# Performance work log

Hardware: AMD Instinct MI355X
Metric: run time of the kernel (lower is better)

## Reference

```python
import jax, jax.numpy as jnp
import numpy as np

D_MODEL, D_KV, N_HEADS = 1024, 64, 16
NUM_BUCKETS, MAX_DIST = 32, 128
B, S = 2, 2048


def _relative_position_bucket(relative_position, num_buckets=NUM_BUCKETS, max_distance=MAX_DIST):
    # bidirectional=True branch of the TF code
    nb = num_buckets // 2
    n = -relative_position
    ret = (n < 0).astype(jnp.int32) * nb
    n = jnp.abs(n)
    max_exact = nb // 2
    is_small = n < max_exact
    val_if_large = max_exact + (
        jnp.log(n.astype(jnp.float32) / max_exact)
        / np.log(max_distance / max_exact)
        * (nb - max_exact)
    ).astype(jnp.int32)
    val_if_large = jnp.minimum(val_if_large, nb - 1)
    return ret + jnp.where(is_small, n, val_if_large)


def compute_bias(rel_emb, qlen, klen):
    ctx = jnp.arange(qlen)[:, None]
    mem = jnp.arange(klen)[None, :]
    rp_bucket = _relative_position_bucket(mem - ctx)  # [q, k]
    values = rel_emb[rp_bucket]                       # [q, k, h]
    return jnp.transpose(values, (2, 0, 1))[None]     # [1, h, q, k]


def setup_inputs() -> dict:
    key = jax.random.key(0)
    ks = jax.random.split(key, 6)
    sc = 1.0 / np.sqrt(D_MODEL)
    return {
        "inputs": jax.random.normal(ks[0], (B, S, D_MODEL), jnp.float32),
        "Wq": jax.random.normal(ks[1], (D_MODEL, N_HEADS * D_KV), jnp.float32) * sc,
        "Wk": jax.random.normal(ks[2], (D_MODEL, N_HEADS * D_KV), jnp.float32) * sc,
        "Wv": jax.random.normal(ks[3], (D_MODEL, N_HEADS * D_KV), jnp.float32) * sc,
        "Wo": jax.random.normal(ks[4], (N_HEADS * D_KV, D_MODEL), jnp.float32) * sc,
        "rel_emb": jax.random.normal(ks[5], (NUM_BUCKETS, N_HEADS), jnp.float32),
    }


def reference(inputs, Wq, Wk, Wv, Wo, rel_emb):
    bs, qlen, _ = inputs.shape

    def split_heads(x):
        return jnp.transpose(x.reshape(bs, -1, N_HEADS, D_KV), (0, 2, 1, 3))

    q = split_heads(inputs @ Wq)  # [b, h, s, d]
    k = split_heads(inputs @ Wk)
    v = split_heads(inputs @ Wv)

    position_bias = compute_bias(rel_emb, qlen, qlen)      # [1, h, q, k]
    scores = jnp.einsum('bnqd,bnkd->bnqk', q, k) + position_bias  # NOTE: no 1/sqrt(d) scaling (T5 style)
    attn = jax.nn.softmax(scores, axis=-1)
    hidden = jnp.einsum('bnqk,bnkd->bnqd', attn, v)
    hidden = jnp.transpose(hidden, (0, 2, 1, 3)).reshape(bs, qlen, N_HEADS * D_KV)
    return hidden @ Wo
```

## Files before the change

### kernel.cpp

```cpp
#include <hip/hip_runtime.h>


typedef __attribute__((ext_vector_type(8))) short s16x8;
typedef __attribute__((ext_vector_type(4))) float f32x4;
typedef __attribute__((ext_vector_type(16))) float f32x16;
typedef __attribute__((ext_vector_type(2))) unsigned int u32x2;

#if __has_builtin(__builtin_amdgcn_exp2f)
#define EXP2(x) __builtin_amdgcn_exp2f(x)
#else
#define EXP2(x) exp2f(x)
#endif

__device__ __forceinline__ unsigned short f2bf(float f) {
  unsigned int u = __float_as_uint(f);
  u = (u + 0x7fffu + ((u >> 16) & 1u)) >> 16;
  return (unsigned short)u;
}

__device__ __forceinline__ unsigned cvtpk(float lo, float hi) {
  unsigned r;
  asm("v_cvt_pk_bf16_f32 %0, %1, %2" : "=v"(r) : "v"(lo), "v"(hi));
  return r;
}

#define GLD16(g, l)                                              \
  __builtin_amdgcn_global_load_lds(                              \
      (const __attribute__((address_space(1))) void*)(g),        \
      (__attribute__((address_space(3))) void*)(l), 16, 0, 0)

__global__ __launch_bounds__(256) void cvt_lin(const float* __restrict__ in,
                                               unsigned short* __restrict__ out,
                                               int n4) {
  int i = blockIdx.x * 256 + threadIdx.x;
  int stride = gridDim.x * 256;
  for (; i < n4; i += stride) {
    float4 v = ((const float4*)in)[i];
    ushort4 o;
    o.x = f2bf(v.x); o.y = f2bf(v.y); o.z = f2bf(v.z); o.w = f2bf(v.w);
    ((ushort4*)out)[i] = o;
  }
}

__global__ __launch_bounds__(256) void cvt_prep(const float* __restrict__ W0,
                                                const float* __restrict__ W1,
                                                const float* __restrict__ W2,
                                                const float* __restrict__ W3,
                                                const float* __restrict__ rel,
                                                unsigned short* __restrict__ Dqkv,
                                                unsigned short* __restrict__ Do_,
                                                float* __restrict__ tab) {
  const int z = blockIdx.z;
  if (z == 4) {
    int idx = (blockIdx.y * 32 + blockIdx.x) * 256 + threadIdx.x;
    if (idx >= 16 * 4096) return;
    int h = idx >> 12, di = idx & 4095;
    int delta = di - 2047;
    int n = -delta;
    int ret = (n < 0) ? 16 : 0;
    n = n < 0 ? -n : n;
    int bucket;
    if (n < 8) {
      bucket = ret + n;
    } else {
      float lf = (float)log((double)n * 0.125);
      float f = lf / 2.772588722239781f * 8.0f;
      int v = 8 + (int)f;
      bucket = ret + (v < 15 ? v : 15);
    }
    tab[idx] = rel[bucket * 16 + h] * 1.4426950408889634f;
    return;
  }
  const float* W = (z == 0) ? W0 : (z == 1) ? W1 : (z == 2) ? W2 : W3;
  unsigned short* WT = (z < 3) ? (Dqkv + (size_t)z * 1024 * 1024) : Do_;
  __shared__ float t[32][33];
  int n0 = blockIdx.x * 32, k0 = blockIdx.y * 32;
  int tx = threadIdx.x & 31, ty = threadIdx.x >> 5;
#pragma unroll
  for (int i = 0; i < 32; i += 8)
    t[ty + i][tx] = W[(size_t)(k0 + ty + i) * 1024 + n0 + tx];
  __syncthreads();
#pragma unroll
  for (int i = 0; i < 32; i += 8)
    WT[(size_t)(n0 + ty + i) * 1024 + k0 + tx] = f2bf(t[tx][ty + i]);
}

__global__ __launch_bounds__(256, 2) void gemm_qkv(
    const unsigned short* __restrict__ A, const unsigned short* __restrict__ BT,
    unsigned short* __restrict__ O0, unsigned short* __restrict__ O1,
    unsigned short* __restrict__ O2) {
  __shared__ __align__(16) unsigned short aT[128 * 64];
  __shared__ __align__(16) unsigned short bT[128 * 64];
  const int tid = threadIdx.x;
  const int lane = tid & 63, w = tid >> 6;
  const int l15 = lane & 15, l4 = lane >> 4;
  const int m0 = blockIdx.y * 128, n0 = blockIdx.x * 128;
  const int wr = w >> 1, wc = w & 1;

  const f32x4 fzero = {0.f, 0.f, 0.f, 0.f};
  f32x4 acc[4][4];
#pragma unroll
  for (int i = 0; i < 4; ++i)
#pragma unroll
    for (int j = 0; j < 4; ++j) acc[i][j] = fzero;

  for (int k0 = 0; k0 < 1024; k0 += 64) {
#pragma unroll
    for (int p = 0; p < 4; ++p) {
      int slot = (p * 4 + w) * 64 + lane;
      int row = slot >> 3, s = slot & 7;
      int ks = (s ^ (row & 7)) << 3;
      GLD16(A + (size_t)(m0 + row) * 1024 + k0 + ks, (char*)aT + (p * 4 + w) * 1024);
      GLD16(BT + (size_t)(n0 + row) * 1024 + k0 + ks, (char*)bT + (p * 4 + w) * 1024);
    }
    __syncthreads();
#pragma unroll
    for (int kk = 0; kk < 2; ++kk) {
      int slotk = kk * 4 + l4;
      s16x8 af[4], bfr[4];
#pragma unroll
      for (int mi = 0; mi < 4; ++mi) {
        int row = wr * 64 + mi * 16 + l15;
        af[mi] = *(const s16x8*)(aT + row * 64 + ((slotk ^ (row & 7)) << 3));
      }
#pragma unroll
      for (int nj = 0; nj < 4; ++nj) {
        int row = wc * 64 + nj * 16 + l15;
        bfr[nj] = *(const s16x8*)(bT + row * 64 + ((slotk ^ (row & 7)) << 3));
      }
      __builtin_amdgcn_s_setprio(1);
#pragma unroll
      for (int mi = 0; mi < 4; ++mi)
#pragma unroll
        for (int nj = 0; nj < 4; ++nj)
          acc[mi][nj] = __builtin_amdgcn_mfma_f32_16x16x32_bf16(af[mi], bfr[nj], acc[mi][nj], 0, 0, 0);
      __builtin_amdgcn_s_setprio(0);
    }
    __syncthreads();
  }

#pragma unroll
  for (int mi = 0; mi < 4; ++mi)
#pragma unroll
    for (int nj = 0; nj < 4; ++nj)
#pragma unroll
      for (int r = 0; r < 4; ++r) {
        int row = m0 + wr * 64 + mi * 16 + l4 * 4 + r;
        int col = n0 + wc * 64 + nj * 16 + l15;
        int which = col >> 10;
        int cc = col & 1023;
        int b = row >> 11, s2 = row & 2047, hh = cc >> 6, d = cc & 63;
        if (which == 0)
          O0[((size_t)((b * 16 + hh) * 2048 + s2)) * 64 + d] =
              f2bf(acc[mi][nj][r] * 1.4426950408889634f);
        else if (which == 1)
          O1[((size_t)((b * 16 + hh) * 2048 + s2)) * 64 + d] = f2bf(acc[mi][nj][r]);
        else
          O2[((size_t)((b * 16 + hh) * 64 + d)) * 2048 + s2] = f2bf(acc[mi][nj][r]);
      }
}

__global__ __launch_bounds__(256, 2) void gemm_op(
    const unsigned short* __restrict__ A, const unsigned short* __restrict__ BT,
    float* __restrict__ O) {
  __shared__ __align__(16) unsigned short aT[128 * 64];
  __shared__ __align__(16) unsigned short bT[64 * 64];
  const int tid = threadIdx.x;
  const int lane = tid & 63, w = tid >> 6;
  const int l15 = lane & 15, l4 = lane >> 4;
  const int m0 = blockIdx.y * 128, n0 = blockIdx.x * 64;
  const int wr = w >> 1, wc = w & 1;

  const f32x4 fzero = {0.f, 0.f, 0.f, 0.f};
  f32x4 acc[4][2];
#pragma unroll
  for (int i = 0; i < 4; ++i)
#pragma unroll
    for (int j = 0; j < 2; ++j) acc[i][j] = fzero;

  for (int k0 = 0; k0 < 1024; k0 += 64) {
#pragma unroll
    for (int p = 0; p < 4; ++p) {
      int slot = (p * 4 + w) * 64 + lane;
      int row = slot >> 3, s = slot & 7;
      int ks = (s ^ (row & 7)) << 3;
      GLD16(A + (size_t)(m0 + row) * 1024 + k0 + ks, (char*)aT + (p * 4 + w) * 1024);
    }
#pragma unroll
    for (int p = 0; p < 2; ++p) {
      int slot = (p * 4 + w) * 64 + lane;
      int row = slot >> 3, s = slot & 7;
      int ks = (s ^ (row & 7)) << 3;
      GLD16(BT + (size_t)(n0 + row) * 1024 + k0 + ks, (char*)bT + (p * 4 + w) * 1024);
    }
    __syncthreads();
#pragma unroll
    for (int kk = 0; kk < 2; ++kk) {
      int slotk = kk * 4 + l4;
      s16x8 af[4], bfr[2];
#pragma unroll
      for (int mi = 0; mi < 4; ++mi) {
        int row = wr * 64 + mi * 16 + l15;
        af[mi] = *(const s16x8*)(aT + row * 64 + ((slotk ^ (row & 7)) << 3));
      }
#pragma unroll
      for (int nj = 0; nj < 2; ++nj) {
        int row = wc * 32 + nj * 16 + l15;
        bfr[nj] = *(const s16x8*)(bT + row * 64 + ((slotk ^ (row & 7)) << 3));
      }
      __builtin_amdgcn_s_setprio(1);
#pragma unroll
      for (int mi = 0; mi < 4; ++mi)
#pragma unroll
        for (int nj = 0; nj < 2; ++nj)
          acc[mi][nj] = __builtin_amdgcn_mfma_f32_16x16x32_bf16(af[mi], bfr[nj], acc[mi][nj], 0, 0, 0);
      __builtin_amdgcn_s_setprio(0);
    }
    __syncthreads();
  }

#pragma unroll
  for (int mi = 0; mi < 4; ++mi)
#pragma unroll
    for (int nj = 0; nj < 2; ++nj)
#pragma unroll
      for (int r = 0; r < 4; ++r) {
        int row = m0 + wr * 64 + mi * 16 + l4 * 4 + r;
        int col = n0 + wc * 32 + nj * 16 + l15;
        O[(size_t)row * 1024 + col] = acc[mi][nj][r];
      }
}

__global__ __launch_bounds__(512, 2) void attn_k(
    const unsigned short* __restrict__ Q,
    const unsigned short* __restrict__ K,
    const unsigned short* __restrict__ VT,
    const float* __restrict__ btab,
    unsigned short* __restrict__ H) {
  __shared__ __align__(16) char smem[65536];
  const int tid = threadIdx.x;
  const int lane = tid & 63, w = tid >> 6;
  const int l31 = lane & 31, l5 = lane >> 5;
  const int half = w >> 2;
  const int q0 = blockIdx.x * 128 + (w & 3) * 32;
  const int bh = blockIdx.y, h = bh & 15, b = bh >> 4;
  const unsigned short* Qp = Q + (size_t)bh * 2048 * 64;
  const unsigned short* Kp = K + (size_t)bh * 2048 * 64;
  const unsigned short* Vp = VT + (size_t)bh * 64 * 2048;
  const float* btq = btab + h * 4096 + 2047 - (q0 + l31) + 4 * l5 + half * 1024;

#define STAGE(buf, kvv)                                                              \
  {                                                                                  \
    int row_ = tid >> 3, s_ = tid & 7;                                               \
    int ks_ = (s_ ^ (row_ & 7)) << 3;                                                \
    GLD16(Kp + (size_t)((kvv) + row_) * 64 + ks_, smem + (buf) * 8192 + tid * 16);   \
    GLD16(Kp + (size_t)(1024 + (kvv) + row_) * 64 + ks_,                             \
          smem + 32768 + (buf) * 8192 + tid * 16);                                   \
    GLD16(Vp + (size_t)row_ * 2048 + (kvv) + ks_,                                    \
          smem + 16384 + (buf) * 8192 + tid * 16);                                   \
    GLD16(Vp + (size_t)row_ * 2048 + 1024 + (kvv) + ks_,                             \
          smem + 16384 + 32768 + (buf) * 8192 + tid * 16);                           \
  }

  s16x8 qf[4];
#pragma unroll
  for (int ks = 0; ks < 4; ++ks)
    qf[ks] = *(const s16x8*)(Qp + (size_t)(q0 + l31) * 64 + ks * 16 + l5 * 8);

  f32x16 oacc[2];
#pragma unroll
  for (int r = 0; r < 16; ++r) { oacc[0][r] = 0.f; oacc[1][r] = 0.f; }
  float s4[4] = {0.f, 0.f, 0.f, 0.f};

  STAGE(0, 0);
  __syncthreads();
  int cur = 0;
  const char* kbase = smem + half * 32768;
  const char* vbase = smem + half * 32768 + 16384;

#define BODY(KVV)                                                                    \
  {                                                                                  \
    const int kvv = (KVV);                                                           \
    if (kvv + 64 < 1024) STAGE(cur ^ 1, kvv + 64);                                   \
                               \
    f32x16 st[2];                                                                    \
    _Pragma("unroll") for (int t = 0; t < 2; ++t)                                    \
      _Pragma("unroll") for (int r = 0; r < 16; ++r)                                 \
        st[t][r] = btq[kvv + t * 32 + (r & 3) + 8 * (r >> 2)];                       \
    const char* kl = kbase + cur * 8192;                                             \
    __builtin_amdgcn_s_setprio(1);                                                   \
    _Pragma("unroll") for (int ks = 0; ks < 4; ++ks) {                               \
      int sl = ks * 2 + l5;                                                          \
      int sw = (sl ^ (l31 & 7)) << 4;                                                \
      s16x8 ka0 = *(const s16x8*)(kl + l31 * 128 + sw);                              \
      s16x8 ka1 = *(const s16x8*)(kl + (32 + l31) * 128 + sw);                       \
      st[0] = __builtin_amdgcn_mfma_f32_32x32x16_bf16(ka0, qf[ks], st[0], 0, 0, 0);  \
      st[1] = __builtin_amdgcn_mfma_f32_32x32x16_bf16(ka1, qf[ks], st[1], 0, 0, 0);  \
    }                                                                                \
    __builtin_amdgcn_s_setprio(0);                                                   \
    _Pragma("unroll") for (int t = 0; t < 2; ++t)                                    \
      _Pragma("unroll") for (int r = 0; r < 16; ++r) {                               \
        float p_ = EXP2(st[t][r]);                                                   \
        st[t][r] = p_;                                                               \
        s4[r & 3] += p_;                                                             \
      }                                                                              \
    s16x8 pb[4];                                                                     \
    _Pragma("unroll") for (int t = 0; t < 2; ++t)                                    \
      _Pragma("unroll") for (int hh = 0; hh < 2; ++hh) {                             \
        unsigned cA = cvtpk(st[t][hh * 8 + 0], st[t][hh * 8 + 1]);                   \
        unsigned cB = cvtpk(st[t][hh * 8 + 2], st[t][hh * 8 + 3]);                   \
        unsigned cC = cvtpk(st[t][hh * 8 + 4], st[t][hh * 8 + 5]);                   \
        unsigned cD = cvtpk(st[t][hh * 8 + 6], st[t][hh * 8 + 7]);                   \
        u32x2 s1 = __builtin_amdgcn_permlane32_swap(cA, cC, false, false);           \
        u32x2 s2 = __builtin_amdgcn_permlane32_swap(cB, cD, false, false);           \
        union { unsigned u[4]; s16x8 v; } pu;                                        \
        pu.u[0] = s1.x; pu.u[1] = s2.x; pu.u[2] = s1.y; pu.u[3] = s2.y;              \
        pb[t * 2 + hh] = pu.v;                                                       \
      }                                                                              \
    const char* vl = vbase + cur * 8192;                                             \
    __builtin_amdgcn_s_setprio(1);                                                   \
    _Pragma("unroll") for (int ks2 = 0; ks2 < 4; ++ks2) {                            \
      int sl = ks2 * 2 + l5;                                                         \
      int sw = (sl ^ (l31 & 7)) << 4;                                                \
      s16x8 va0 = *(const s16x8*)(vl + l31 * 128 + sw);                              \
      s16x8 va1 = *(const s16x8*)(vl + (32 + l31) * 128 + sw);                       \
      oacc[0] = __builtin_amdgcn_mfma_f32_32x32x16_bf16(va0, pb[ks2], oacc[0], 0, 0, 0); \
      oacc[1] = __builtin_amdgcn_mfma_f32_32x32x16_bf16(va1, pb[ks2], oacc[1], 0, 0, 0); \
    }                                                                                \
    __builtin_amdgcn_s_setprio(0);                                                   \
    __syncthreads();                                                                 \
    cur ^= 1;                                                                        \
  }

  for (int s = 0; s < 16; ++s) BODY(s * 64);
#undef BODY
#undef STAGE

  float sum = (s4[0] + s4[1]) + (s4[2] + s4[3]);
  u32x2 rs = __builtin_amdgcn_permlane32_swap(__float_as_uint(sum), __float_as_uint(sum), false, false);
  float lsum = __uint_as_float(rs.x) + __uint_as_float(rs.y);

  float* comb = (float*)smem;
  if (w >= 4) {
    float* p = comb + ((w - 4) * 64 + lane) * 34;
#pragma unroll
    for (int r = 0; r < 16; ++r) { p[r] = oacc[0][r]; p[16 + r] = oacc[1][r]; }
    p[32] = lsum;
  }
  __syncthreads();
  if (w < 4) {
    const float* p = comb + (w * 64 + lane) * 34;
#pragma unroll
    for (int r = 0; r < 16; ++r) { oacc[0][r] += p[r]; oacc[1][r] += p[16 + r]; }
    float inv = 1.0f / (lsum + p[32]);
    size_t hb = (((size_t)(b * 2048 + q0 + l31)) * 1024 + h * 64 + 4 * l5) * 2;
#pragma unroll
    for (int nd = 0; nd < 2; ++nd)
#pragma unroll
      for (int g = 0; g < 4; ++g) {
        unsigned w0 = cvtpk(oacc[nd][g * 4 + 0] * inv, oacc[nd][g * 4 + 1] * inv);
        unsigned w1 = cvtpk(oacc[nd][g * 4 + 2] * inv, oacc[nd][g * 4 + 3] * inv);
        unsigned long long pk8 = (unsigned long long)w0 | ((unsigned long long)w1 << 32);
        *(unsigned long long*)((char*)H + hb + (nd * 32 + 8 * g) * 2) = pk8;
      }
  }
}

extern "C" void kernel_launch(void* const* d_in, const int* in_sizes, int n_in,
                              void* d_out, int out_size, void* d_ws, size_t ws_size,
                              hipStream_t stream) {
  const float* X   = (const float*)d_in[0];
  const float* Wq  = (const float*)d_in[1];
  const float* Wk  = (const float*)d_in[2];
  const float* Wv  = (const float*)d_in[3];
  const float* Wo  = (const float*)d_in[4];
  const float* rel = (const float*)d_in[5];

  char* ws = (char*)d_ws;
  unsigned short* Xb     = (unsigned short*)(ws);
  unsigned short* Hid    = Xb;
  unsigned short* WqkvT  = (unsigned short*)(ws + (8u << 20));
  unsigned short* WoT    = (unsigned short*)(ws + (14u << 20));
  unsigned short* Qb     = (unsigned short*)(ws + (16u << 20));
  unsigned short* Kb     = (unsigned short*)(ws + (24u << 20));
  unsigned short* VTb    = (unsigned short*)(ws + (32u << 20));
  float* btab            = (float*)(ws + (40u << 20));

  cvt_lin<<<1024, 256, 0, stream>>>(X, Xb, (2 * 2048 * 1024) / 4);
  cvt_prep<<<dim3(32, 32, 5), 256, 0, stream>>>(Wq, Wk, Wv, Wo, rel, WqkvT, WoT, btab);

  gemm_qkv<<<dim3(24, 32), 256, 0, stream>>>(Xb, WqkvT, Qb, Kb, VTb);

  attn_k<<<dim3(16, 32), 512, 0, stream>>>(Qb, Kb, VTb, btab, Hid);

  gemm_op<<<dim3(16, 32), 256, 0, stream>>>(Hid, WoT, (float*)d_out);
}
```

Before: 117.7 us.

## Double-buffer GEMM LDS tiles and read attention K/V directly from global

The two projection GEMMs now use double-buffered LDS tiles, prefetching the next K-slice while computing the current one. This replaces the load-then-sync pattern that stalled on each tile. The attention kernel drops its LDS staging of K and V and each wave reads its fragments directly from global memory. That cuts LDS use and removes the per-iteration barrier, but it relies on cache hits and un-swizzled global loads sitting in the MFMA dependency chain. The GEMM LDS footprint doubles, which may affect occupancy.

```diff
diff --git a/kernel.cpp b/kernel.cpp
--- a/kernel.cpp
+++ b/kernel.cpp
@@ -89,14 +89,27 @@
     const unsigned short* __restrict__ A, const unsigned short* __restrict__ BT,
     unsigned short* __restrict__ O0, unsigned short* __restrict__ O1,
     unsigned short* __restrict__ O2) {
-  __shared__ __align__(16) unsigned short aT[128 * 64];
-  __shared__ __align__(16) unsigned short bT[128 * 64];
+  __shared__ __align__(16) unsigned short aT[2][128 * 64];
+  __shared__ __align__(16) unsigned short bT[2][128 * 64];
   const int tid = threadIdx.x;
   const int lane = tid & 63, w = tid >> 6;
   const int l15 = lane & 15, l4 = lane >> 4;
   const int m0 = blockIdx.y * 128, n0 = blockIdx.x * 128;
   const int wr = w >> 1, wc = w & 1;
 
+#define QSTAGE(buf, k0)                                                             \
+  {                                                                                 \
+    _Pragma("unroll") for (int p = 0; p < 4; ++p) {                                 \
+      int slot = (p * 4 + w) * 64 + lane;                                           \
+      int row = slot >> 3, s = slot & 7;                                            \
+      int ks = (s ^ (row & 7)) << 3;                                                \
+      GLD16(A + (size_t)(m0 + row) * 1024 + (k0) + ks,                              \
+            (char*)aT[buf] + (p * 4 + w) * 1024);                                   \
+      GLD16(BT + (size_t)(n0 + row) * 1024 + (k0) + ks,                             \
+            (char*)bT[buf] + (p * 4 + w) * 1024);                                   \
+    }                                                                               \
+  }
+
   const f32x4 fzero = {0.f, 0.f, 0.f, 0.f};
   f32x4 acc[4][4];
 #pragma unroll
@@ -104,16 +117,11 @@
 #pragma unroll
     for (int j = 0; j < 4; ++j) acc[i][j] = fzero;
 
+  QSTAGE(0, 0);
+  __syncthreads();
+  int cur = 0;
   for (int k0 = 0; k0 < 1024; k0 += 64) {
-#pragma unroll
-    for (int p = 0; p < 4; ++p) {
-      int slot = (p * 4 + w) * 64 + lane;
-      int row = slot >> 3, s = slot & 7;
-      int ks = (s ^ (row & 7)) << 3;
-      GLD16(A + (size_t)(m0 + row) * 1024 + k0 + ks, (char*)aT + (p * 4 + w) * 1024);
-      GLD16(BT + (size_t)(n0 + row) * 1024 + k0 + ks, (char*)bT + (p * 4 + w) * 1024);
-    }
-    __syncthreads();
+    if (k0 + 64 < 1024) QSTAGE(cur ^ 1, k0 + 64);
 #pragma unroll
     for (int kk = 0; kk < 2; ++kk) {
       int slotk = kk * 4 + l4;
@@ -121,12 +129,12 @@
 #pragma unroll
       for (int mi = 0; mi < 4; ++mi) {
         int row = wr * 64 + mi * 16 + l15;
-        af[mi] = *(const s16x8*)(aT + row * 64 + ((slotk ^ (row & 7)) << 3));
+        af[mi] = *(const s16x8*)(aT[cur] + row * 64 + ((slotk ^ (row & 7)) << 3));
       }
 #pragma unroll
       for (int nj = 0; nj < 4; ++nj) {
         int row = wc * 64 + nj * 16 + l15;
-        bfr[nj] = *(const s16x8*)(bT + row * 64 + ((slotk ^ (row & 7)) << 3));
+        bfr[nj] = *(const s16x8*)(bT[cur] + row * 64 + ((slotk ^ (row & 7)) << 3));
       }
       __builtin_amdgcn_s_setprio(1);
 #pragma unroll
@@ -137,7 +145,9 @@
       __builtin_amdgcn_s_setprio(0);
     }
     __syncthreads();
-  }
+    cur ^= 1;
+  }
+#undef QSTAGE
 
 #pragma unroll
   for (int mi = 0; mi < 4; ++mi)
@@ -163,14 +173,32 @@
 __global__ __launch_bounds__(256, 2) void gemm_op(
     const unsigned short* __restrict__ A, const unsigned short* __restrict__ BT,
     float* __restrict__ O) {
-  __shared__ __align__(16) unsigned short aT[128 * 64];
-  __shared__ __align__(16) unsigned short bT[64 * 64];
+  __shared__ __align__(16) unsigned short aT[2][128 * 64];
+  __shared__ __align__(16) unsigned short bT[2][64 * 64];
   const int tid = threadIdx.x;
   const int lane = tid & 63, w = tid >> 6;
   const int l15 = lane & 15, l4 = lane >> 4;
   const int m0 = blockIdx.y * 128, n0 = blockIdx.x * 64;
   const int wr = w >> 1, wc = w & 1;
 
+#define OSTAGE(buf, k0)                                                             \
+  {                                                                                 \
+    _Pragma("unroll") for (int p = 0; p < 4; ++p) {                                 \
+      int slot = (p * 4 + w) * 64 + lane;                                           \
+      int row = slot >> 3, s = slot & 7;                                            \
+      int ks = (s ^ (row & 7)) << 3;                                                \
+      GLD16(A + (size_t)(m0 + row) * 1024 + (k0) + ks,                              \
+            (char*)aT[buf] + (p * 4 + w) * 1024);                                   \
+    }                                                                               \
+    _Pragma("unroll") for (int p = 0; p < 2; ++p) {                                 \
+      int slot = (p * 4 + w) * 64 + lane;                                           \
+      int row = slot >> 3, s = slot & 7;                                            \
+      int ks = (s ^ (row & 7)) << 3;                                                \
+      GLD16(BT + (size_t)(n0 + row) * 1024 + (k0) + ks,                             \
+            (char*)bT[buf] + (p * 4 + w) * 1024);                                   \
+    }                                                                               \
+  }
+
   const f32x4 fzero = {0.f, 0.f, 0.f, 0.f};
   f32x4 acc[4][2];
 #pragma unroll
@@ -178,22 +206,11 @@
 #pragma unroll
     for (int j = 0; j < 2; ++j) acc[i][j] = fzero;
 
+  OSTAGE(0, 0);
+  __syncthreads();
+  int cur = 0;
   for (int k0 = 0; k0 < 1024; k0 += 64) {
-#pragma unroll
-    for (int p = 0; p < 4; ++p) {
-      int slot = (p * 4 + w) * 64 + lane;
-      int row = slot >> 3, s = slot & 7;
-      int ks = (s ^ (row & 7)) << 3;
-      GLD16(A + (size_t)(m0 + row) * 1024 + k0 + ks, (char*)aT + (p * 4 + w) * 1024);
-    }
-#pragma unroll
-    for (int p = 0; p < 2; ++p) {
-      int slot = (p * 4 + w) * 64 + lane;
-      int row = slot >> 3, s = slot & 7;
-      int ks = (s ^ (row & 7)) << 3;
-      GLD16(BT + (size_t)(n0 + row) * 1024 + k0 + ks, (char*)bT + (p * 4 + w) * 1024);
-    }
-    __syncthreads();
+    if (k0 + 64 < 1024) OSTAGE(cur ^ 1, k0 + 64);
 #pragma unroll
     for (int kk = 0; kk < 2; ++kk) {
       int slotk = kk * 4 + l4;
@@ -201,12 +218,12 @@
 #pragma unroll
       for (int mi = 0; mi < 4; ++mi) {
         int row = wr * 64 + mi * 16 + l15;
-        af[mi] = *(const s16x8*)(aT + row * 64 + ((slotk ^ (row & 7)) << 3));
+        af[mi] = *(const s16x8*)(aT[cur] + row * 64 + ((slotk ^ (row & 7)) << 3));
       }
 #pragma unroll
       for (int nj = 0; nj < 2; ++nj) {
         int row = wc * 32 + nj * 16 + l15;
-        bfr[nj] = *(const s16x8*)(bT + row * 64 + ((slotk ^ (row & 7)) << 3));
+        bfr[nj] = *(const s16x8*)(bT[cur] + row * 64 + ((slotk ^ (row & 7)) << 3));
       }
       __builtin_amdgcn_s_setprio(1);
 #pragma unroll
@@ -217,7 +234,9 @@
       __builtin_amdgcn_s_setprio(0);
     }
     __syncthreads();
-  }
+    cur ^= 1;
+  }
+#undef OSTAGE
 
 #pragma unroll
   for (int mi = 0; mi < 4; ++mi)
@@ -237,7 +256,7 @@
     const unsigned short* __restrict__ VT,
     const float* __restrict__ btab,
     unsigned short* __restrict__ H) {
-  __shared__ __align__(16) char smem[65536];
+  __shared__ __align__(16) char smem[36864];
   const int tid = threadIdx.x;
   const int lane = tid & 63, w = tid >> 6;
   const int l31 = lane & 31, l5 = lane >> 5;
@@ -245,22 +264,9 @@
   const int q0 = blockIdx.x * 128 + (w & 3) * 32;
   const int bh = blockIdx.y, h = bh & 15, b = bh >> 4;
   const unsigned short* Qp = Q + (size_t)bh * 2048 * 64;
-  const unsigned short* Kp = K + (size_t)bh * 2048 * 64;
-  const unsigned short* Vp = VT + (size_t)bh * 64 * 2048;
+  const unsigned short* Kp = K + (size_t)bh * 2048 * 64 + (size_t)half * 1024 * 64;
+  const unsigned short* Vp = VT + (size_t)bh * 64 * 2048 + half * 1024;
   const float* btq = btab + h * 4096 + 2047 - (q0 + l31) + 4 * l5 + half * 1024;
-
-#define STAGE(buf, kvv)                                                              \
-  {                                                                                  \
-    int row_ = tid >> 3, s_ = tid & 7;                                               \
-    int ks_ = (s_ ^ (row_ & 7)) << 3;                                                \
-    GLD16(Kp + (size_t)((kvv) + row_) * 64 + ks_, smem + (buf) * 8192 + tid * 16);   \
-    GLD16(Kp + (size_t)(1024 + (kvv) + row_) * 64 + ks_,                             \
-          smem + 32768 + (buf) * 8192 + tid * 16);                                   \
-    GLD16(Vp + (size_t)row_ * 2048 + (kvv) + ks_,                                    \
-          smem + 16384 + (buf) * 8192 + tid * 16);                                   \
-    GLD16(Vp + (size_t)row_ * 2048 + 1024 + (kvv) + ks_,                             \
-          smem + 16384 + 32768 + (buf) * 8192 + tid * 16);                           \
-  }
 
   s16x8 qf[4];
 #pragma unroll
@@ -272,69 +278,61 @@
   for (int r = 0; r < 16; ++r) { oacc[0][r] = 0.f; oacc[1][r] = 0.f; }
   float s4[4] = {0.f, 0.f, 0.f, 0.f};
 
-  STAGE(0, 0);
-  __syncthreads();
-  int cur = 0;
-  const char* kbase = smem + half * 32768;
-  const char* vbase = smem + half * 32768 + 16384;
-
-#define BODY(KVV)                                                                    \
-  {                                                                                  \
-    const int kvv = (KVV);                                                           \
-    if (kvv + 64 < 1024) STAGE(cur ^ 1, kvv + 64);                                   \
-                               \
-    f32x16 st[2];                                                                    \
-    _Pragma("unroll") for (int t = 0; t < 2; ++t)                                    \
-      _Pragma("unroll") for (int r = 0; r < 16; ++r)                                 \
-        st[t][r] = btq[kvv + t * 32 + (r & 3) + 8 * (r >> 2)];                       \
-    const char* kl = kbase + cur * 8192;                                             \
-    __builtin_amdgcn_s_setprio(1);                                                   \
-    _Pragma("unroll") for (int ks = 0; ks < 4; ++ks) {                               \
-      int sl = ks * 2 + l5;                                                          \
-      int sw = (sl ^ (l31 & 7)) << 4;                                                \
-      s16x8 ka0 = *(const s16x8*)(kl + l31 * 128 + sw);                              \
-      s16x8 ka1 = *(const s16x8*)(kl + (32 + l31) * 128 + sw);                       \
-      st[0] = __builtin_amdgcn_mfma_f32_32x32x16_bf16(ka0, qf[ks], st[0], 0, 0, 0);  \
-      st[1] = __builtin_amdgcn_mfma_f32_32x32x16_bf16(ka1, qf[ks], st[1], 0, 0, 0);  \
-    }                                                                                \
-    __builtin_amdgcn_s_setprio(0);                                                   \
-    _Pragma("unroll") for (int t = 0; t < 2; ++t)                                    \
-      _Pragma("unroll") for (int r = 0; r < 16; ++r) {                               \
-        float p_ = EXP2(st[t][r]);                                                   \
-        st[t][r] = p_;                                                               \
-        s4[r & 3] += p_;                                                             \
-      }                                                                              \
-    s16x8 pb[4];                                                                     \
-    _Pragma("unroll") for (int t = 0; t < 2; ++t)                                    \
-      _Pragma("unroll") for (int hh = 0; hh < 2; ++hh) {                             \
-        unsigned cA = cvtpk(st[t][hh * 8 + 0], st[t][hh * 8 + 1]);                   \
-        unsigned cB = cvtpk(st[t][hh * 8 + 2], st[t][hh * 8 + 3]);                   \
-        unsigned cC = cvtpk(st[t][hh * 8 + 4], st[t][hh * 8 + 5]);                   \
-        unsigned cD = cvtpk(st[t][hh * 8 + 6], st[t][hh * 8 + 7]);                   \
-        u32x2 s1 = __builtin_amdgcn_permlane32_swap(cA, cC, false, false);           \
-        u32x2 s2 = __builtin_amdgcn_permlane32_swap(cB, cD, false, false);           \
-        union { unsigned u[4]; s16x8 v; } pu;                                        \
-        pu.u[0] = s1.x; pu.u[1] = s2.x; pu.u[2] = s1.y; pu.u[3] = s2.y;              \
-        pb[t * 2 + hh] = pu.v;                                                       \
-      }                                                                              \
-    const char* vl = vbase + cur * 8192;                                             \
-    __builtin_amdgcn_s_setprio(1);                                                   \
-    _Pragma("unroll") for (int ks2 = 0; ks2 < 4; ++ks2) {                            \
-      int sl = ks2 * 2 + l5;                                                         \
-      int sw = (sl ^ (l31 & 7)) << 4;                                                \
-      s16x8 va0 = *(const s16x8*)(vl + l31 * 128 + sw);                              \
-      s16x8 va1 = *(const s16x8*)(vl + (32 + l31) * 128 + sw);                       \
-      oacc[0] = __builtin_amdgcn_mfma_f32_32x32x16_bf16(va0, pb[ks2], oacc[0], 0, 0, 0); \
-      oacc[1] = __builtin_amdgcn_mfma_f32_32x32x16_bf16(va1, pb[ks2], oacc[1], 0, 0, 0); \
-    }                                                                                \
-    __builtin_amdgcn_s_setprio(0);                                                   \
-    __syncthreads();                                                                 \
-    cur ^= 1;                                                                        \
-  }
-
-  for (int s = 0; s < 16; ++s) BODY(s * 64);
-#undef BODY
-#undef STAGE
+  for (int kvv = 0; kvv < 1024; kvv += 64) {
+    f32x16 st[2];
+#pragma unroll
+    for (int t = 0; t < 2; ++t)
+#pragma unroll
+      for (int r = 0; r < 16; ++r)
+        st[t][r] = btq[kvv + t * 32 + (r & 3) + 8 * (r >> 2)];
+
+    const unsigned short* kp = Kp + (size_t)kvv * 64;
+    __builtin_amdgcn_s_setprio(1);
+#pragma unroll
+    for (int ks = 0; ks < 4; ++ks) {
+      s16x8 ka0 = *(const s16x8*)(kp + (size_t)l31 * 64 + ks * 16 + l5 * 8);
+      s16x8 ka1 = *(const s16x8*)(kp + (size_t)(32 + l31) * 64 + ks * 16 + l5 * 8);
+      st[0] = __builtin_amdgcn_mfma_f32_32x32x16_bf16(ka0, qf[ks], st[0], 0, 0, 0);
+      st[1] = __builtin_amdgcn_mfma_f32_32x32x16_bf16(ka1, qf[ks], st[1], 0, 0, 0);
+    }
+    __builtin_amdgcn_s_setprio(0);
+
+#pragma unroll
+    for (int t = 0; t < 2; ++t)
+#pragma unroll
+      for (int r = 0; r < 16; ++r) {
+        float p_ = EXP2(st[t][r]);
+        st[t][r] = p_;
+        s4[r & 3] += p_;
+      }
+
+    s16x8 pb[4];
+#pragma unroll
+    for (int t = 0; t < 2; ++t)
+#pragma unroll
+      for (int hh = 0; hh < 2; ++hh) {
+        unsigned cA = cvtpk(st[t][hh * 8 + 0], st[t][hh * 8 + 1]);
+        unsigned cB = cvtpk(st[t][hh * 8 + 2], st[t][hh * 8 + 3]);
+        unsigned cC = cvtpk(st[t][hh * 8 + 4], st[t][hh * 8 + 5]);
+        unsigned cD = cvtpk(st[t][hh * 8 + 6], st[t][hh * 8 + 7]);
+        u32x2 s1 = __builtin_amdgcn_permlane32_swap(cA, cC, false, false);
+        u32x2 s2 = __builtin_amdgcn_permlane32_swap(cB, cD, false, false);
+        union { unsigned u[4]; s16x8 v; } pu;
+        pu.u[0] = s1.x; pu.u[1] = s2.x; pu.u[2] = s1.y; pu.u[3] = s2.y;
+        pb[t * 2 + hh] = pu.v;
+      }
+
+    const unsigned short* vp = Vp + kvv;
+    __builtin_amdgcn_s_setprio(1);
+#pragma unroll
+    for (int ks2 = 0; ks2 < 4; ++ks2) {
+      s16x8 va0 = *(const s16x8*)(vp + (size_t)l31 * 2048 + ks2 * 16 + l5 * 8);
+      s16x8 va1 = *(const s16x8*)(vp + (size_t)(32 + l31) * 2048 + ks2 * 16 + l5 * 8);
+      oacc[0] = __builtin_amdgcn_mfma_f32_32x32x16_bf16(va0, pb[ks2], oacc[0], 0, 0, 0);
+      oacc[1] = __builtin_amdgcn_mfma_f32_32x32x16_bf16(va1, pb[ks2], oacc[1], 0, 0, 0);
+    }
+    __builtin_amdgcn_s_setprio(0);
+  }
 
   float sum = (s4[0] + s4[1]) + (s4[2] + s4[3]);
   u32x2 rs = __builtin_amdgcn_permlane32_swap(__float_as_uint(sum), __float_as_uint(sum), false, false);
```

Result: slower. 217.4 us (+84.7%).
